# Optimization experiments

Measured on AMD Instinct MI355X. Metric: run time of the kernel, lower is better.

Reference implementation:

```python
import jax, jax.numpy as jnp
import numpy as np

B, C, IC, H, W = 4, 256, 128, 64, 64
EPS = 1e-5  # BatchNorm eps (eval mode, running stats)


def conv_bn(x, w, b, gamma, beta, mean, var, relu):
    # 1x1 conv == channel contraction; BN in eval mode (affine w/ running stats)
    y = jnp.einsum('oc,bchw->bohw', w, x) + b[None, :, None, None]
    scale = gamma * jax.lax.rsqrt(var + EPS)
    shift = beta - mean * scale
    y = y * scale[None, :, None, None] + shift[None, :, None, None]
    return jax.nn.relu(y) if relu else y


def setup_inputs() -> dict:
    key = jax.random.key(0)
    ks = jax.random.split(key, 32)

    def branch(i, co, ci):
        return dict(
            w=jax.random.normal(ks[i], (co, ci), jnp.float32) * 0.05,
            b=jax.random.normal(ks[i + 1], (co,), jnp.float32) * 0.05,
            gamma=jax.random.uniform(ks[i + 2], (co,), jnp.float32, 0.5, 1.5),
            beta=jax.random.normal(ks[i + 3], (co,), jnp.float32) * 0.05,
            mean=jax.random.normal(ks[i + 4], (co,), jnp.float32) * 0.05,
            var=jax.random.uniform(ks[i + 5], (co,), jnp.float32, 0.5, 1.5),
        )

    g = branch(0, IC, C)
    th = branch(6, IC, C)
    ph = branch(12, IC, C)
    wo = branch(18, C, IC)
    inp = {'x': jax.random.normal(ks[24], (B, C, H, W), jnp.float32)}
    for pre, p in (('g', g), ('th', th), ('ph', ph), ('w', wo)):
        for k, v in p.items():
            inp[f'{pre}_{k}'] = v
    return inp


def reference(x, g_w, g_b, g_gamma, g_beta, g_mean, g_var,
              th_w, th_b, th_gamma, th_beta, th_mean, th_var,
              ph_w, ph_b, ph_gamma, ph_beta, ph_mean, ph_var,
              w_w, w_b, w_gamma, w_beta, w_mean, w_var):
    b, c, h, w = x.shape
    ic = g_w.shape[0]
    g_x = conv_bn(x, g_w, g_b, g_gamma, g_beta, g_mean, g_var, True).reshape(b, ic, h * w)     # [b,ic,n]
    theta = conv_bn(x, th_w, th_b, th_gamma, th_beta, th_mean, th_var, True).reshape(b, ic, h * w)
    phi = conv_bn(x, ph_w, ph_b, ph_gamma, ph_beta, ph_mean, ph_var, True).reshape(b, ic, h * w)
    # unscaled attention over flattened spatial positions
    f = jnp.einsum('bcn,bcm->bnm', theta, phi)     # [b,n,n]
    a = jax.nn.softmax(f, axis=2)
    y = jnp.einsum('bnm,bcm->bcn', a, g_x)         # [b,ic,n]
    y = y.reshape(b, ic, h, w)
    y = conv_bn(y, w_w, w_b, w_gamma, w_beta, w_mean, w_var, False)
    return y + x
```

## Files before the change

kernel.cpp:

```cpp
#include <hip/hip_runtime.h>
#include <math.h>

typedef __attribute__((ext_vector_type(8))) short short8;
typedef __attribute__((ext_vector_type(8))) _Float16 half8;
typedef __attribute__((ext_vector_type(4))) float f32x4;

#define NSP 4096
#define CIN 256
#define ICH 128
#define LOG2E 1.44269504088896f

__device__ __forceinline__ unsigned short f2h(float x){
  union { _Float16 h; unsigned short u; } v; v.h = (_Float16)x; return v.u;
}
__device__ __forceinline__ float h2f(unsigned short u){
  union { _Float16 h; unsigned short u; } v; v.u = u; return (float)v.h;
}
__device__ __forceinline__ unsigned pk2h(float a, float b){
  union { __fp16 __attribute__((ext_vector_type(2))) v; unsigned u; } r;
  r.v = __builtin_amdgcn_cvt_pkrtz(a, b);
  return r.u;
}
__device__ __forceinline__ float fexp2(float x){
  float r;
  asm("v_exp_f32 %0, %1" : "=v"(r) : "v"(x));
  return r;
}
__device__ __forceinline__ int swz(int row, int e){ return e ^ ((row & 7) << 3); }

__device__ __forceinline__ f32x4 mfmah(short8 a, short8 b, f32x4 c){
  union { short8 s; half8 h; } ua, ub; ua.s = a; ub.s = b;
  return __builtin_amdgcn_mfma_f32_16x16x32_f16(ua.h, ub.h, c, 0, 0, 0);
}

__device__ __forceinline__ void st4h(unsigned short* p, unsigned short a, unsigned short b,
                                     unsigned short c, unsigned short d){
  ushort4 v; v.x=a; v.y=b; v.z=c; v.w=d;
  *(ushort4*)p = v;
}

__device__ __forceinline__ void gload_lds16(const unsigned short* g, unsigned short* l){
  __builtin_amdgcn_global_load_lds(
      (const __attribute__((address_space(1))) unsigned int*)g,
      (__attribute__((address_space(3))) unsigned int*)l, 16, 0, 0);
}

__device__ __forceinline__ void stage_nc(const unsigned short* gbase, unsigned short* lds,
                                         int w, int l){
  #pragma unroll
  for (int i=0;i<4;++i){
    int rl = 16*w + 4*i + (l>>4);
    int eg = ((l&15)*8) ^ ((rl&7)<<3);
    gload_lds16(gbase + (size_t)rl*128 + eg, lds + w*2048 + i*512);
  }
}

__device__ __forceinline__ int kperm(int q){
  return ((q>>4)&1)*4 + ((q>>2)&3)*8 + (q&3);
}

__global__ __launch_bounds__(256) void conv_fused_k(
    const float* __restrict__ x,
    const float* __restrict__ w0, const float* __restrict__ b0,
    const float* __restrict__ ga0, const float* __restrict__ be0,
    const float* __restrict__ me0, const float* __restrict__ va0,
    const float* __restrict__ w1, const float* __restrict__ b1,
    const float* __restrict__ ga1, const float* __restrict__ be1,
    const float* __restrict__ me1, const float* __restrict__ va1,
    const float* __restrict__ w2, const float* __restrict__ b2,
    const float* __restrict__ ga2, const float* __restrict__ be2,
    const float* __restrict__ me2, const float* __restrict__ va2,
    unsigned short* __restrict__ outg, unsigned short* __restrict__ outt,
    unsigned short* __restrict__ outp)
{
  const int b = blockIdx.z, nt = blockIdx.x, ot = blockIdx.y;
  const int n0 = nt*64, o0 = ot*64;
  const int t = threadIdx.x, w = t>>6, l = t&63;
  __shared__ unsigned short xs[64][64];
  __shared__ unsigned short ws[3][64][64];
  __shared__ float sc_s[3][64], sh_s[3][64];
  if (t < 64){
    int o = o0 + t;
    float s0 = ga0[o]*rsqrtf(va0[o]+1e-5f);
    sc_s[0][t]=s0; sh_s[0][t]=be0[o]-me0[o]*s0+b0[o]*s0;
    float s1 = ga1[o]*rsqrtf(va1[o]+1e-5f);
    sc_s[1][t]=s1*LOG2E; sh_s[1][t]=(be1[o]-me1[o]*s1+b1[o]*s1)*LOG2E;
    float s2 = ga2[o]*rsqrtf(va2[o]+1e-5f);
    sc_s[2][t]=s2; sh_s[2][t]=be2[o]-me2[o]*s2+b2[o]*s2;
  }
  const f32x4 Z = {0.f,0.f,0.f,0.f};
  f32x4 acc[3][4];
  #pragma unroll
  for (int br=0;br<3;++br) for (int i=0;i<4;++i) acc[br][i] = Z;
  const float* Wt[3] = {w0, w1, w2};

  for (int kc = 0; kc < CIN; kc += 64){
    __syncthreads();
    #pragma unroll
    for (int p = 0; p < 4; ++p){
      int cw = p*16 + (t>>4);
      int q4 = (t&15)*4;
      float4 xv = *(const float4*)(x + ((size_t)b*CIN + kc + cw)*NSP + n0 + q4);
      float xa[4] = {xv.x, xv.y, xv.z, xv.w};
      #pragma unroll
      for (int i=0;i<4;++i){
        int r = q4 + i;
        xs[r][swz(r, cw)] = f2h(xa[i]);
      }
      #pragma unroll
      for (int br=0;br<3;++br){
        float4 wv = *(const float4*)(Wt[br] + (size_t)(o0 + cw)*CIN + kc + q4);
        int cs = swz(cw, q4);
        st4h(&ws[br][cw][cs], f2h(wv.x), f2h(wv.y), f2h(wv.z), f2h(wv.w));
      }
    }
    __syncthreads();
    #pragma unroll
    for (int kf = 0; kf < 2; ++kf){
      int ko = kf*32 + (l>>4)*8;
      int wr = 16*w + (l&15);
      short8 wf0 = *(const short8*)&ws[0][wr][swz(wr, ko)];
      short8 wf1 = *(const short8*)&ws[1][wr][swz(wr, ko)];
      short8 wf2 = *(const short8*)&ws[2][wr][swz(wr, ko)];
      #pragma unroll
      for (int nf = 0; nf < 4; ++nf){
        int xr = 16*nf + (l&15);
        short8 xf = *(const short8*)&xs[xr][swz(xr, ko)];
        acc[0][nf] = mfmah(wf0, xf, acc[0][nf]);
        acc[1][nf] = mfmah(xf, wf1, acc[1][nf]);
        acc[2][nf] = mfmah(xf, wf2, acc[2][nf]);
      }
    }
  }
  #pragma unroll
  for (int j=0;j<4;++j){
    int ol = 16*w + (l>>4)*4 + j;
    float s = sc_s[0][ol], sh = sh_s[0][ol];
    #pragma unroll
    for (int nf=0;nf<4;++nf){
      int n = n0 + 16*nf + (l&15);
      int nst = (n & ~31) | kperm(n & 31);
      float v = fmaxf(acc[0][nf][j]*s + sh, 0.f);
      outg[((size_t)b*ICH + o0 + ol)*NSP + nst] = f2h(v);
    }
  }
  {
    int ol = 16*w + (l&15);
    float s1 = sc_s[1][ol], sh1 = sh_s[1][ol];
    float s2 = sc_s[2][ol], sh2 = sh_s[2][ol];
    #pragma unroll
    for (int nf=0; nf<4; ++nf)
      #pragma unroll
      for (int j=0;j<4;++j){
        int n = n0 + 16*nf + (l>>4)*4 + j;
        float v1 = fmaxf(acc[1][nf][j]*s1 + sh1, 0.f);
        float v2 = fmaxf(acc[2][nf][j]*s2 + sh2, 0.f);
        outt[((size_t)b*NSP + n)*ICH + o0 + ol] = f2h(v1);
        outp[((size_t)b*NSP + n)*ICH + o0 + ol] = f2h(v2);
      }
  }
}

template<int SPLITS_T>
__global__ __launch_bounds__(256, 3) void attn_k(
  const unsigned short* __restrict__ thp, const unsigned short* __restrict__ php,
  const unsigned short* __restrict__ gb, unsigned short* __restrict__ ypart,
  float* __restrict__ ml)
{
  constexpr int TPS = 64/SPLITS_T;
  const int bx = blockIdx.x;
  const int xcd = bx & 7, jj = bx >> 3;
  const int combo = xcd*(SPLITS_T/2) + jj/32;
  const int qt = jj % 32;
  const int b = combo & 3, s = combo >> 2;
  const int n0 = qt*128;
  const int t = threadIdx.x, w = t>>6, l = t&63;

  __shared__ unsigned short kb[2][64][128];
  __shared__ unsigned short vb[128][64];
  unsigned short* vbf = &vb[0][0];

  stage_nc(thp + ((size_t)b*NSP + n0      )*ICH, &kb[0][0][0], w, l);
  stage_nc(thp + ((size_t)b*NSP + n0 + 64 )*ICH, &kb[1][0][0], w, l);
  __syncthreads();
  short8 qf0[4], qf1[4];
  {
    int qr = 16*w + (l&15);
    #pragma unroll
    for (int kf=0;kf<4;++kf){
      int ko = kf*32 + (l>>4)*8;
      qf0[kf] = *(const short8*)&kb[0][qr][swz(qr, ko)];
      qf1[kf] = *(const short8*)&kb[1][qr][swz(qr, ko)];
    }
  }
  __syncthreads();

  const f32x4 Z = {0.f,0.f,0.f,0.f};
  f32x4 oa0[8], oa1[8];
  #pragma unroll
  for (int i=0;i<8;++i){ oa0[i]=Z; oa1[i]=Z; }
  float m0r = -1e30f, m1r = -1e30f;
  float l0r = 0.f, l1r = 0.f;
  unsigned pk0[8], pk1[8];

  const int tile0 = s*TPS;

  const unsigned short* kp[4];
  const unsigned short* vp[4];
  {
    const unsigned short* kbase = php + ((size_t)b*NSP + tile0*64)*ICH;
    const unsigned short* vbase = gb + (size_t)b*ICH*NSP + tile0*64;
    #pragma unroll
    for (int i=0;i<4;++i){
      int rl = 16*w + 4*i + (l>>4);
      int eg = ((l&15)*8) ^ ((rl&7)<<3);
      kp[i] = kbase + (size_t)rl*128 + eg;
      int cl = 32*w + 8*i + (l>>3);
      int me = ((l&7)*8) ^ ((cl&7)<<3);
      vp[i] = vbase + (size_t)cl*NSP + me;
    }
  }
  {
    unsigned short* kd = &kb[0][0][0] + w*2048;
    #pragma unroll
    for (int i=0;i<4;++i){
      gload_lds16(kp[i], kd + i*512); kp[i] += 64*ICH;
    }
  }
  __syncthreads();
  int cur = 0;

  for (int it = 0; it < TPS; ++it){
    {
      unsigned short* vd = vbf + w*2048;
      #pragma unroll
      for (int i=0;i<4;++i){
        gload_lds16(vp[i], vd + i*512); vp[i] += 64;
      }
    }
    if (it < TPS-1){
      unsigned short* kd = &kb[cur^1][0][0] + w*2048;
      #pragma unroll
      for (int i=0;i<4;++i){
        gload_lds16(kp[i], kd + i*512); kp[i] += 64*ICH;
      }
    }

    f32x4 f0[4], f1[4];
    #pragma unroll
    for (int i=0;i<4;++i){ f0[i]=Z; f1[i]=Z; }
    __builtin_amdgcn_s_setprio(1);
    #pragma unroll
    for (int mf=0; mf<4; ++mf){
      int kr = 16*mf + (l&15);
      #pragma unroll
      for (int kf=0; kf<4; ++kf){
        short8 bh = *(const short8*)&kb[cur][kr][swz(kr, kf*32 + (l>>4)*8)];
        f0[mf] = mfmah(bh, qf0[kf], f0[mf]);
        f1[mf] = mfmah(bh, qf1[kf], f1[mf]);
      }
    }
    __builtin_amdgcn_s_setprio(0);

    #pragma unroll
    for (int h=0; h<2; ++h){
      f32x4* f = h ? f1 : f0;
      float& mr = h ? m1r : m0r;
      float& lr = h ? l1r : l0r;
      f32x4* oa = h ? oa1 : oa0;
      unsigned* pk = h ? pk1 : pk0;
      float a0 = fmaxf(fmaxf(f[0][0], f[0][1]), fmaxf(f[0][2], f[0][3]));
      float a1 = fmaxf(fmaxf(f[1][0], f[1][1]), fmaxf(f[1][2], f[1][3]));
      float a2 = fmaxf(fmaxf(f[2][0], f[2][1]), fmaxf(f[2][2], f[2][3]));
      float a3 = fmaxf(fmaxf(f[3][0], f[3][1]), fmaxf(f[3][2], f[3][3]));
      float mx = fmaxf(fmaxf(a0, a1), fmaxf(a2, a3));
      mx = fmaxf(mx, __shfl_xor(mx, 16));
      mx = fmaxf(mx, __shfl_xor(mx, 32));
      if (__any(mx - mr > 11.5f)){
        float mn = fmaxf(mr, mx);
        float al = fexp2(mr - mn);
        mr = mn; lr *= al;
        #pragma unroll
        for (int j=0;j<4;++j){
          float alj = __shfl(al, (l>>4)*4 + j);
          #pragma unroll
          for (int cf=0;cf<8;++cf) oa[cf][j] *= alj;
        }
      }
      float s0 = 0.f, s1 = 0.f, s2 = 0.f, s3 = 0.f;
      #pragma unroll
      for (int mf=0;mf<4;++mf){
        float p0 = fexp2(f[mf][0] - mr);
        float p1 = fexp2(f[mf][1] - mr);
        float p2 = fexp2(f[mf][2] - mr);
        float p3 = fexp2(f[mf][3] - mr);
        pk[2*mf+0] = pk2h(p0, p1);
        pk[2*mf+1] = pk2h(p2, p3);
        s0 += p0; s1 += p1; s2 += p2; s3 += p3;
      }
      lr += (s0 + s1) + (s2 + s3);
    }

    if (it < TPS-1)
      asm volatile("s_waitcnt vmcnt(4)" ::: "memory");
    else
      asm volatile("s_waitcnt vmcnt(0)" ::: "memory");
    __builtin_amdgcn_s_barrier();
    __builtin_amdgcn_sched_barrier(0);

    __builtin_amdgcn_s_setprio(1);
    {
      int g8 = (l>>4)*8;
      #pragma unroll
      for (int mk=0;mk<2;++mk){
        union { unsigned u[4]; short8 s8; } a0u, a1u;
        #pragma unroll
        for (int q=0;q<4;++q){ a0u.u[q] = pk0[4*mk+q]; a1u.u[q] = pk1[4*mk+q]; }
        #pragma unroll
        for (int cf=0;cf<8;++cf){
          int vr = 16*cf + (l&15);
          short8 bv = *(const short8*)&vbf[vr*64 + swz(vr, mk*32 + g8)];
          oa0[cf] = mfmah(a0u.s8, bv, oa0[cf]);
          oa1[cf] = mfmah(a1u.s8, bv, oa1[cf]);
        }
      }
    }
    __builtin_amdgcn_s_setprio(0);

    __syncthreads();
    cur ^= 1;
  }

  #pragma unroll
  for (int h=0; h<2; ++h){
    float mr = h ? m1r : m0r;
    float lr = h ? l1r : l0r;
    f32x4* oa = h ? oa1 : oa0;
    lr += __shfl_xor(lr, 16);
    lr += __shfl_xor(lr, 32);
    float invl = 1.f / lr;
    #pragma unroll
    for (int j=0;j<4;++j){
      float inv = __shfl(invl, (l>>4)*4 + j);
      int n = n0 + h*64 + 16*w + (l>>4)*4 + j;
      #pragma unroll
      for (int cf=0;cf<8;++cf){
        int c = 16*cf + (l&15);
        ypart[(((size_t)s*4 + b)*NSP + n)*ICH + c] = f2h(oa[cf][j]*inv);
      }
    }
    if (l < 16){
      int n = n0 + h*64 + 16*w + l;
      ml[(((size_t)s*4 + b)*NSP + n)*2 + 0] = mr;
      ml[(((size_t)s*4 + b)*NSP + n)*2 + 1] = lr;
    }
  }
}

template<int SPL>
__global__ __launch_bounds__(256) void final_k(
  const unsigned short* __restrict__ ypart, const float* __restrict__ ml,
  const float* __restrict__ x, const float* __restrict__ Wm,
  const float* __restrict__ bias, const float* __restrict__ gamma,
  const float* __restrict__ beta, const float* __restrict__ mean,
  const float* __restrict__ var, float* __restrict__ out)
{
  const int b = blockIdx.z, ot = blockIdx.y, nt = blockIdx.x;
  const int n0 = nt*64, o0 = ot*64;
  const int t = threadIdx.x, w = t>>6, l = t&63;
  __shared__ unsigned short ys[64][128];
  __shared__ unsigned short w2s[64][128];
  __shared__ float wc[SPL][64];
  __shared__ float sc_s[64], sh_s[64];
  if (t < 64){
    int o = o0 + t;
    float s = gamma[o]*rsqrtf(var[o]+1e-5f);
    sc_s[t]=s; sh_s[t]=beta[o]-mean[o]*s+bias[o]*s;
  } else if (t < 128){
    int r = t - 64, n = n0 + r;
    float mv[SPL], lv[SPL];
    #pragma unroll
    for (int s=0;s<SPL;++s){
      mv[s] = ml[(((size_t)s*4 + b)*NSP + n)*2 + 0];
      lv[s] = ml[(((size_t)s*4 + b)*NSP + n)*2 + 1];
    }
    float M = mv[0];
    #pragma unroll
    for (int s=1;s<SPL;++s) M = fmaxf(M, mv[s]);
    float wsum = 0.f, wv[SPL];
    #pragma unroll
    for (int s=0;s<SPL;++s){ wv[s] = lv[s]*exp2f(mv[s]-M); wsum += wv[s]; }
    float inv = 1.f/wsum;
    #pragma unroll
    for (int s=0;s<SPL;++s) wc[s][r] = wv[s]*inv;
  }
  __syncthreads();
  #pragma unroll
  for (int p=0;p<4;++p){
    int id = p*256 + t, r = id>>4, c8 = (id&15)*8;
    float accv[8] = {0,0,0,0,0,0,0,0};
    #pragma unroll
    for (int s=0;s<SPL;++s){
      short8 v = *(const short8*)(ypart + (((size_t)s*4 + b)*NSP + n0 + r)*ICH + c8);
      float wgt = wc[s][r];
      #pragma unroll
      for (int i=0;i<8;++i) accv[i] += wgt * h2f(((unsigned short*)&v)[i]);
    }
    unsigned short hv[8];
    #pragma unroll
    for (int i=0;i<8;++i) hv[i] = f2h(accv[i]);
    *(short8*)&ys[r][swz(r,c8)] = *(short8*)hv;

    float4 u0 = *(const float4*)(Wm + (size_t)(o0 + r)*ICH + c8);
    float4 u1 = *(const float4*)(Wm + (size_t)(o0 + r)*ICH + c8 + 4);
    unsigned short wh[8] = {f2h(u0.x),f2h(u0.y),f2h(u0.z),f2h(u0.w),
                            f2h(u1.x),f2h(u1.y),f2h(u1.z),f2h(u1.w)};
    *(short8*)&w2s[r][swz(r,c8)] = *(short8*)wh;
  }
  __syncthreads();
  const f32x4 Z = {0.f,0.f,0.f,0.f};
  f32x4 acc[4];
  for (int i=0;i<4;++i) acc[i]=Z;
  #pragma unroll
  for (int kf=0;kf<4;++kf){
    int ko = kf*32 + (l>>4)*8;
    int wr = 16*w + (l&15);
    short8 a = *(const short8*)&w2s[wr][swz(wr,ko)];
    #pragma unroll
    for (int nf=0;nf<4;++nf){
      int yr = 16*nf + (l&15);
      short8 bb = *(const short8*)&ys[yr][swz(yr,ko)];
      acc[nf] = mfmah(a, bb, acc[nf]);
    }
  }
  #pragma unroll
  for (int j=0;j<4;++j){
    int ol = 16*w + (l>>4)*4 + j;
    float s = sc_s[ol], sh = sh_s[ol];
    #pragma unroll
    for (int nf=0;nf<4;++nf){
      int n = n0 + 16*nf + (l&15);
      size_t idx = ((size_t)b*CIN + o0 + ol)*NSP + n;
      out[idx] = acc[nf][j]*s + sh + x[idx];
    }
  }
}

extern "C" void kernel_launch(void* const* d_in, const int* in_sizes, int n_in,
                              void* d_out, int out_size, void* d_ws, size_t ws_size,
                              hipStream_t stream){
  const float* x    = (const float*)d_in[0];
  const float* g_w  = (const float*)d_in[1];
  const float* g_b  = (const float*)d_in[2];
  const float* g_ga = (const float*)d_in[3];
  const float* g_be = (const float*)d_in[4];
  const float* g_me = (const float*)d_in[5];
  const float* g_va = (const float*)d_in[6];
  const float* t_w  = (const float*)d_in[7];
  const float* t_b  = (const float*)d_in[8];
  const float* t_ga = (const float*)d_in[9];
  const float* t_be = (const float*)d_in[10];
  const float* t_me = (const float*)d_in[11];
  const float* t_va = (const float*)d_in[12];
  const float* p_w  = (const float*)d_in[13];
  const float* p_b  = (const float*)d_in[14];
  const float* p_ga = (const float*)d_in[15];
  const float* p_be = (const float*)d_in[16];
  const float* p_me = (const float*)d_in[17];
  const float* p_va = (const float*)d_in[18];
  const float* w_w  = (const float*)d_in[19];
  const float* w_b  = (const float*)d_in[20];
  const float* w_ga = (const float*)d_in[21];
  const float* w_be = (const float*)d_in[22];
  const float* w_me = (const float*)d_in[23];
  const float* w_va = (const float*)d_in[24];

  char* ws = (char*)d_ws;
  const size_t SEG = (size_t)4*NSP*ICH*sizeof(unsigned short);
  const size_t MLSZ8 = (size_t)8*4*NSP*2*sizeof(float);
  const size_t NEED8 = 3*SEG + 8*SEG + MLSZ8;

  unsigned short* th_t  = (unsigned short*)(ws);
  unsigned short* ph_t  = (unsigned short*)(ws + SEG);
  unsigned short* g_cn  = (unsigned short*)(ws + 2*SEG);
  unsigned short* ypart = (unsigned short*)(ws + 3*SEG);

  dim3 blk(256,1,1);
  conv_fused_k<<<dim3(64,2,4), blk, 0, stream>>>(
      x,
      g_w, g_b, g_ga, g_be, g_me, g_va,
      t_w, t_b, t_ga, t_be, t_me, t_va,
      p_w, p_b, p_ga, p_be, p_me, p_va,
      g_cn, th_t, ph_t);

  if (ws_size >= NEED8){
    float* mlb = (float*)(ws + 3*SEG + 8*SEG);
    attn_k<8><<<dim3(1024,1,1), blk, 0, stream>>>(th_t, ph_t, g_cn, ypart, mlb);
    final_k<8><<<dim3(64,4,4), blk, 0, stream>>>(ypart, mlb, x, w_w, w_b, w_ga, w_be, w_me, w_va, (float*)d_out);
  } else {
    float* mlb = (float*)(ws + 3*SEG + 4*SEG);
    attn_k<4><<<dim3(512,1,1), blk, 0, stream>>>(th_t, ph_t, g_cn, ypart, mlb);
    final_k<4><<<dim3(64,4,4), blk, 0, stream>>>(ypart, mlb, x, w_w, w_b, w_ga, w_be, w_me, w_va, (float*)d_out);
  }
}
```

Measured before the change: 82.62 us.

## Software-pipeline attention QK^T one tile ahead with double-buffered K and V

Restructures the attention loop so the QK^T MFMAs for the next key tile are issued before the softmax and PV work on the current tile. K and V get double-buffered LDS and deeper async prefetch, with explicit vmcnt waits per stage. The split count is fixed at 4 (512 blocks, launch bounds down to 2 waves/SIMD), dropping the 8-split path. This aims to hide exp/softmax latency and memory loads behind matrix work, at the cost of more registers and LDS, lower occupancy and less parallelism.

```diff
diff --git a/kernel.cpp b/kernel.cpp
--- a/kernel.cpp
+++ b/kernel.cpp
@@ -8,6 +8,8 @@
 #define NSP 4096
 #define CIN 256
 #define ICH 128
+#define SPLITS 4
+#define TPS 16
 #define LOG2E 1.44269504088896f
 
 __device__ __forceinline__ unsigned short f2h(float x){
@@ -161,27 +163,28 @@
   }
 }
 
-template<int SPLITS_T>
-__global__ __launch_bounds__(256, 3) void attn_k(
+__global__ __launch_bounds__(256, 2) void attn_k(
   const unsigned short* __restrict__ thp, const unsigned short* __restrict__ php,
   const unsigned short* __restrict__ gb, unsigned short* __restrict__ ypart,
   float* __restrict__ ml)
 {
-  constexpr int TPS = 64/SPLITS_T;
   const int bx = blockIdx.x;
   const int xcd = bx & 7, jj = bx >> 3;
-  const int combo = xcd*(SPLITS_T/2) + jj/32;
-  const int qt = jj % 32;
+  const int combo = xcd*2 + (jj>>5);
+  const int qt = jj & 31;
   const int b = combo & 3, s = combo >> 2;
   const int n0 = qt*128;
   const int t = threadIdx.x, w = t>>6, l = t&63;
 
-  __shared__ unsigned short kb[2][64][128];
-  __shared__ unsigned short vb[128][64];
-  unsigned short* vbf = &vb[0][0];
-
-  stage_nc(thp + ((size_t)b*NSP + n0      )*ICH, &kb[0][0][0], w, l);
-  stage_nc(thp + ((size_t)b*NSP + n0 + 64 )*ICH, &kb[1][0][0], w, l);
+  __shared__ unsigned short kbuf[2][8192];
+  __shared__ unsigned short vbuf[2][8192];
+  unsigned short* kb0 = kbuf[0];
+  unsigned short* kb1 = kbuf[1];
+  unsigned short* vb0 = vbuf[0];
+  unsigned short* vb1 = vbuf[1];
+
+  stage_nc(thp + ((size_t)b*NSP + n0      )*ICH, kb0, w, l);
+  stage_nc(thp + ((size_t)b*NSP + n0 + 64 )*ICH, kb1, w, l);
   __syncthreads();
   short8 qf0[4], qf1[4];
   {
@@ -189,8 +192,8 @@
     #pragma unroll
     for (int kf=0;kf<4;++kf){
       int ko = kf*32 + (l>>4)*8;
-      qf0[kf] = *(const short8*)&kb[0][qr][swz(qr, ko)];
-      qf1[kf] = *(const short8*)&kb[1][qr][swz(qr, ko)];
+      qf0[kf] = *(const short8*)&kb0[qr*128 + swz(qr, ko)];
+      qf1[kf] = *(const short8*)&kb1[qr*128 + swz(qr, ko)];
     }
   }
   __syncthreads();
@@ -202,6 +205,7 @@
   float m0r = -1e30f, m1r = -1e30f;
   float l0r = 0.f, l1r = 0.f;
   unsigned pk0[8], pk1[8];
+  f32x4 fa0[4], fa1[4], fb0[4], fb1[4];
 
   const int tile0 = s*TPS;
 
@@ -221,50 +225,72 @@
     }
   }
   {
-    unsigned short* kd = &kb[0][0][0] + w*2048;
-    #pragma unroll
-    for (int i=0;i<4;++i){
-      gload_lds16(kp[i], kd + i*512); kp[i] += 64*ICH;
-    }
-  }
-  __syncthreads();
-  int cur = 0;
-
-  for (int it = 0; it < TPS; ++it){
-    {
-      unsigned short* vd = vbf + w*2048;
-      #pragma unroll
-      for (int i=0;i<4;++i){
-        gload_lds16(vp[i], vd + i*512); vp[i] += 64;
-      }
-    }
-    if (it < TPS-1){
-      unsigned short* kd = &kb[cur^1][0][0] + w*2048;
-      #pragma unroll
-      for (int i=0;i<4;++i){
-        gload_lds16(kp[i], kd + i*512); kp[i] += 64*ICH;
-      }
-    }
-
-    f32x4 f0[4], f1[4];
-    #pragma unroll
-    for (int i=0;i<4;++i){ f0[i]=Z; f1[i]=Z; }
-    __builtin_amdgcn_s_setprio(1);
-    #pragma unroll
-    for (int mf=0; mf<4; ++mf){
-      int kr = 16*mf + (l&15);
-      #pragma unroll
-      for (int kf=0; kf<4; ++kf){
-        short8 bh = *(const short8*)&kb[cur][kr][swz(kr, kf*32 + (l>>4)*8)];
-        f0[mf] = mfmah(bh, qf0[kf], f0[mf]);
-        f1[mf] = mfmah(bh, qf1[kf], f1[mf]);
-      }
-    }
-    __builtin_amdgcn_s_setprio(0);
-
+    unsigned short* kd = kb0 + w*2048;
+    unsigned short* vd = vb0 + w*2048;
+    #pragma unroll
+    for (int i=0;i<4;++i){ gload_lds16(kp[i], kd + i*512); kp[i] += 64*ICH; }
+    #pragma unroll
+    for (int i=0;i<4;++i){ gload_lds16(vp[i], vd + i*512); vp[i] += 64; }
+    unsigned short* kd1 = kb1 + w*2048;
+    #pragma unroll
+    for (int i=0;i<4;++i){ gload_lds16(kp[i], kd1 + i*512); kp[i] += 64*ICH; }
+  }
+  asm volatile("s_waitcnt vmcnt(4)" ::: "memory");
+  __builtin_amdgcn_s_barrier();
+  __builtin_amdgcn_sched_barrier(0);
+  #pragma unroll
+  for (int i=0;i<4;++i){ fa0[i]=Z; fa1[i]=Z; }
+  #pragma unroll
+  for (int mf=0; mf<4; ++mf){
+    int kr = 16*mf + (l&15);
+    #pragma unroll
+    for (int kf=0; kf<4; ++kf){
+      short8 bh = *(const short8*)&kb0[kr*128 + swz(kr, kf*32 + (l>>4)*8)];
+      fa0[mf] = mfmah(bh, qf0[kf], fa0[mf]);
+      fa1[mf] = mfmah(bh, qf1[kf], fa1[mf]);
+    }
+  }
+  __builtin_amdgcn_s_barrier();
+
+  auto iter_body = [&](int it, int curc, f32x4* c0, f32x4* c1, f32x4* n0, f32x4* n1){
+    unsigned short* kcur_n = curc ? kb0 : kb1;
+    unsigned short* vcur   = curc ? vb1 : vb0;
+    unsigned short* kfree  = curc ? kb1 : kb0;
+    unsigned short* vfree  = curc ? vb0 : vb1;
+
+    if (it <= TPS-3){
+      unsigned short* kd = kfree + w*2048;
+      #pragma unroll
+      for (int i=0;i<4;++i){ gload_lds16(kp[i], kd + i*512); kp[i] += 64*ICH; }
+    }
+    if (it <= TPS-2){
+      unsigned short* vd = vfree + w*2048;
+      #pragma unroll
+      for (int i=0;i<4;++i){ gload_lds16(vp[i], vd + i*512); vp[i] += 64; }
+    }
+    if (it <= TPS-3)      asm volatile("s_waitcnt vmcnt(8)" ::: "memory");
+    else if (it == TPS-2) asm volatile("s_waitcnt vmcnt(4)" ::: "memory");
+    else                  asm volatile("s_waitcnt vmcnt(0)" ::: "memory");
+    __builtin_amdgcn_s_barrier();
+    __builtin_amdgcn_sched_barrier(0);
+
+    if (it <= TPS-2){
+      #pragma unroll
+      for (int i=0;i<4;++i){ n0[i]=Z; n1[i]=Z; }
+      #pragma unroll
+      for (int mf=0; mf<4; ++mf){
+        int kr = 16*mf + (l&15);
+        #pragma unroll
+        for (int kf=0; kf<4; ++kf){
+          short8 bh = *(const short8*)&kcur_n[kr*128 + swz(kr, kf*32 + (l>>4)*8)];
+          n0[mf] = mfmah(bh, qf0[kf], n0[mf]);
+          n1[mf] = mfmah(bh, qf1[kf], n1[mf]);
+        }
+      }
+    }
     #pragma unroll
     for (int h=0; h<2; ++h){
-      f32x4* f = h ? f1 : f0;
+      f32x4* f = h ? c1 : c0;
       float& mr = h ? m1r : m0r;
       float& lr = h ? l1r : l0r;
       f32x4* oa = h ? oa1 : oa0;
@@ -301,13 +327,6 @@
       lr += (s0 + s1) + (s2 + s3);
     }
 
-    if (it < TPS-1)
-      asm volatile("s_waitcnt vmcnt(4)" ::: "memory");
-    else
-      asm volatile("s_waitcnt vmcnt(0)" ::: "memory");
-    __builtin_amdgcn_s_barrier();
-    __builtin_amdgcn_sched_barrier(0);
-
     __builtin_amdgcn_s_setprio(1);
     {
       int g8 = (l>>4)*8;
@@ -319,7 +338,7 @@
         #pragma unroll
         for (int cf=0;cf<8;++cf){
           int vr = 16*cf + (l&15);
-          short8 bv = *(const short8*)&vbf[vr*64 + swz(vr, mk*32 + g8)];
+          short8 bv = *(const short8*)&vcur[vr*64 + swz(vr, mk*32 + g8)];
           oa0[cf] = mfmah(a0u.s8, bv, oa0[cf]);
           oa1[cf] = mfmah(a1u.s8, bv, oa1[cf]);
         }
@@ -327,8 +346,13 @@
     }
     __builtin_amdgcn_s_setprio(0);
 
-    __syncthreads();
-    cur ^= 1;
+    __builtin_amdgcn_s_barrier();
+  };
+
+  #pragma unroll 1
+  for (int i2 = 0; i2 < TPS; i2 += 2){
+    iter_body(i2,   0, fa0, fa1, fb0, fb1);
+    iter_body(i2+1, 1, fb0, fb1, fa0, fa1);
   }
 
   #pragma unroll
@@ -477,13 +501,11 @@
 
   char* ws = (char*)d_ws;
   const size_t SEG = (size_t)4*NSP*ICH*sizeof(unsigned short);
-  const size_t MLSZ8 = (size_t)8*4*NSP*2*sizeof(float);
-  const size_t NEED8 = 3*SEG + 8*SEG + MLSZ8;
-
   unsigned short* th_t  = (unsigned short*)(ws);
   unsigned short* ph_t  = (unsigned short*)(ws + SEG);
   unsigned short* g_cn  = (unsigned short*)(ws + 2*SEG);
   unsigned short* ypart = (unsigned short*)(ws + 3*SEG);
+  float*          mlb   = (float*)(ws + 3*SEG + SPLITS*SEG);
 
   dim3 blk(256,1,1);
   conv_fused_k<<<dim3(64,2,4), blk, 0, stream>>>(
@@ -492,14 +514,6 @@
       t_w, t_b, t_ga, t_be, t_me, t_va,
       p_w, p_b, p_ga, p_be, p_me, p_va,
       g_cn, th_t, ph_t);
-
-  if (ws_size >= NEED8){
-    float* mlb = (float*)(ws + 3*SEG + 8*SEG);
-    attn_k<8><<<dim3(1024,1,1), blk, 0, stream>>>(th_t, ph_t, g_cn, ypart, mlb);
-    final_k<8><<<dim3(64,4,4), blk, 0, stream>>>(ypart, mlb, x, w_w, w_b, w_ga, w_be, w_me, w_va, (float*)d_out);
-  } else {
-    float* mlb = (float*)(ws + 3*SEG + 4*SEG);
-    attn_k<4><<<dim3(512,1,1), blk, 0, stream>>>(th_t, ph_t, g_cn, ypart, mlb);
-    final_k<4><<<dim3(64,4,4), blk, 0, stream>>>(ypart, mlb, x, w_w, w_b, w_ga, w_be, w_me, w_va, (float*)d_out);
-  }
-}
+  attn_k<<<dim3(512,1,1), blk, 0, stream>>>(th_t, ph_t, g_cn, ypart, mlb);
+  final_k<SPLITS><<<dim3(64,4,4), blk, 0, stream>>>(ypart, mlb, x, w_w, w_b, w_ga, w_be, w_me, w_va, (float*)d_out);
+}
```

Result: faster. 79.02 us (-4.4%).
